# Performance work log

Hardware: AMD Instinct MI355X
Metric: run time of the kernel (lower is better)

## Reference

```python
import jax, jax.numpy as jnp
import numpy as np

S = 14
L_COORD = 5.0
L_NOOBJ = 0.5


def setup_inputs() -> dict:
    key = jax.random.key(0)
    k1, k2, k3, k4 = jax.random.split(key, 4)
    N = 4096
    # positive uniforms so sqrt(w), sqrt(h) and IoU areas are well-defined (as in real YOLO outputs)
    pred_tensor = jax.random.uniform(k1, (N, S, S, 30), dtype=jnp.float32, minval=0.01, maxval=1.0)
    target_boxes = jax.random.uniform(k2, (N, S, S, 4), dtype=jnp.float32, minval=0.01, maxval=1.0)
    target_cls = jax.random.uniform(k3, (N, S, S, 20), dtype=jnp.float32)
    has_object_map = jax.random.bernoulli(k4, 0.15, (N, S, S))
    return {"pred_tensor": pred_tensor, "target_boxes": target_boxes,
            "target_cls": target_cls, "has_object_map": has_object_map}


def _xywh2xyxy(b):
    # b: (..., 4) as [cx, cy, w, h]; cx,cy are in grid units -> divide by S
    x, y, w, h = b[..., 0], b[..., 1], b[..., 2], b[..., 3]
    return jnp.stack([x / S - 0.5 * w, y / S - 0.5 * h,
                      x / S + 0.5 * w, y / S + 0.5 * h], axis=-1)


def _iou_pairwise(b1, b2):
    # elementwise IoU between matched boxes (diag of compute_iou), b: (..., 4) xyxy
    lt = jnp.maximum(b1[..., :2], b2[..., :2])
    rb = jnp.minimum(b1[..., 2:], b2[..., 2:])
    wh = jnp.maximum(rb - lt, 0.0)
    inter = wh[..., 0] * wh[..., 1]
    a1 = (b1[..., 2] - b1[..., 0]) * (b1[..., 3] - b1[..., 1])
    a2 = (b2[..., 2] - b2[..., 0]) * (b2[..., 3] - b2[..., 1])
    return inter / (a1 + a2 - inter)


def reference(pred_tensor, target_boxes, target_cls, has_object_map):
    N = pred_tensor.shape[0]
    obj = has_object_map.astype(pred_tensor.dtype)          # (N,S,S)
    noobj = 1.0 - obj

    box1 = pred_tensor[..., 0:5]
    box2 = pred_tensor[..., 5:10]
    pred_cls = pred_tensor[..., 10:]

    # class loss: masked sum-MSE over object cells
    cls_loss = jnp.sum(obj[..., None] * (pred_cls - target_cls) ** 2)

    # no-object loss: confidences of both predictors in non-object cells vs 0
    no_obj_loss = L_NOOBJ * jnp.sum(noobj * (box1[..., 4] ** 2 + box2[..., 4] ** 2))

    # best-of-B selection by IoU against target (elementwise, matched per cell)
    tgt_xyxy = _xywh2xyxy(target_boxes)
    iou1 = _iou_pairwise(_xywh2xyxy(box1[..., :4]), tgt_xyxy)
    iou2 = _iou_pairwise(_xywh2xyxy(box2[..., :4]), tgt_xyxy)
    take1 = iou1 > iou2
    best_iou = jnp.where(take1, iou1, iou2)                  # (N,S,S)
    best_box = jnp.where(take1[..., None], box1, box2)       # (N,S,S,5)

    xy_err = jnp.sum((best_box[..., :2] - target_boxes[..., :2]) ** 2, axis=-1)
    wh_err = jnp.sum((jnp.sqrt(best_box[..., 2:4]) - jnp.sqrt(target_boxes[..., 2:4])) ** 2, axis=-1)
    reg_loss = L_COORD * jnp.sum(obj * (xy_err + wh_err))

    # containing-object confidence loss; target IoU is detached
    contain_loss = jnp.sum(obj * (best_box[..., 4] - jax.lax.stop_gradient(best_iou)) ** 2)

    total = cls_loss + no_obj_loss + contain_loss + reg_loss
    # [total, reg, containing_obj, no_obj, cls], each averaged over batch
    return jnp.stack([total, reg_loss, contain_loss, no_obj_loss, cls_loss]) / N
```

## Files before the change

kernel.cpp:

```cpp
#include <hip/hip_runtime.h>


#define NBATCH   4096
#define SGRID    14
#define CELLS    (NBATCH * SGRID * SGRID)
#define CPB      256
#define NBLK     (CELLS / CPB)
#define L_COORD  5.0f
#define L_NOOBJ  0.5f

__global__ __launch_bounds__(256) void yolo_main(
    const float* __restrict__ pred,
    const float* __restrict__ tbox,
    const float* __restrict__ tcls,
    const int*   __restrict__ objmap,
    float4*      __restrict__ part)
{
    __shared__ float lds_pred[CPB * 30];
    __shared__ float lds_obj[CPB];
    __shared__ float red[4][4];

    const int tid  = threadIdx.x;
    const int blk  = blockIdx.x;
    const int base = blk * CPB;

    {
        const float4* p4  = (const float4*)pred + (size_t)blk * (CPB * 30 / 4);
        float4*       lp4 = (float4*)lds_pred;
        for (int i = tid; i < CPB * 30 / 4; i += 256)
            lp4[i] = p4[i];
    }
    lds_obj[tid] = objmap[base + tid] ? 1.0f : 0.0f;
    __syncthreads();

    float acc_reg = 0.f, acc_cont = 0.f, acc_noobj = 0.f, acc_cls = 0.f;

    {
        const float4* c4 = (const float4*)tcls + (size_t)blk * (CPB * 20 / 4);
        for (int i = tid; i < CPB * 20 / 4; i += 256) {
            float4 t  = c4[i];
            int cell  = i / 5;
            int ch0   = (i - cell * 5) * 4;
            float o   = lds_obj[cell];
            const float* pc = &lds_pred[cell * 30 + 10 + ch0];
            float d0 = pc[0] - t.x, d1 = pc[1] - t.y;
            float d2 = pc[2] - t.z, d3 = pc[3] - t.w;
            acc_cls += o * (d0*d0 + d1*d1 + d2*d2 + d3*d3);
        }
    }

    {
        const float* pp = &lds_pred[tid * 30];
        float x1 = pp[0], y1 = pp[1], w1 = pp[2], h1 = pp[3], c1 = pp[4];
        float x2 = pp[5], y2 = pp[6], w2 = pp[7], h2 = pp[8], c2 = pp[9];
        float o  = lds_obj[tid];
        float no = 1.0f - o;
        acc_noobj = no * (c1*c1 + c2*c2);

        float4 tb = ((const float4*)tbox)[base + tid];
        const float invS = 1.0f / 14.0f;

        float txc = tb.x * invS, tyc = tb.y * invS;
        float tx1 = txc - 0.5f * tb.z, ty1 = tyc - 0.5f * tb.w;
        float tx2 = txc + 0.5f * tb.z, ty2 = tyc + 0.5f * tb.w;
        float ta  = (tx2 - tx1) * (ty2 - ty1);

        float ax1 = x1 * invS - 0.5f * w1, ay1 = y1 * invS - 0.5f * h1;
        float ax2 = x1 * invS + 0.5f * w1, ay2 = y1 * invS + 0.5f * h1;
        float a1  = (ax2 - ax1) * (ay2 - ay1);
        float iw  = fmaxf(fminf(ax2, tx2) - fmaxf(ax1, tx1), 0.f);
        float ih  = fmaxf(fminf(ay2, ty2) - fmaxf(ay1, ty1), 0.f);
        float inter1 = iw * ih;
        float iou1   = inter1 / (a1 + ta - inter1);

        float bx1 = x2 * invS - 0.5f * w2, by1 = y2 * invS - 0.5f * h2;
        float bx2 = x2 * invS + 0.5f * w2, by2 = y2 * invS + 0.5f * h2;
        float a2  = (bx2 - bx1) * (by2 - by1);
        float jw  = fmaxf(fminf(bx2, tx2) - fmaxf(bx1, tx1), 0.f);
        float jh  = fmaxf(fminf(by2, ty2) - fmaxf(by1, ty1), 0.f);
        float inter2 = jw * jh;
        float iou2   = inter2 / (a2 + ta - inter2);

        bool  t1   = iou1 > iou2;
        float bx   = t1 ? x1 : x2,  by = t1 ? y1 : y2;
        float bw   = t1 ? w1 : w2,  bh = t1 ? h1 : h2;
        float bc   = t1 ? c1 : c2;
        float biou = t1 ? iou1 : iou2;

        float dx = bx - tb.x, dy = by - tb.y;
        float dw = sqrtf(bw) - sqrtf(tb.z);
        float dh = sqrtf(bh) - sqrtf(tb.w);
        acc_reg  = o * (dx*dx + dy*dy + dw*dw + dh*dh);
        float dc = bc - biou;
        acc_cont = o * dc * dc;
    }

    #pragma unroll
    for (int off = 32; off > 0; off >>= 1) {
        acc_reg   += __shfl_down(acc_reg,   off);
        acc_cont  += __shfl_down(acc_cont,  off);
        acc_noobj += __shfl_down(acc_noobj, off);
        acc_cls   += __shfl_down(acc_cls,   off);
    }
    const int wave = tid >> 6, lane = tid & 63;
    if (lane == 0) {
        red[wave][0] = acc_reg;
        red[wave][1] = acc_cont;
        red[wave][2] = acc_noobj;
        red[wave][3] = acc_cls;
    }
    __syncthreads();
    if (tid == 0) {
        float4 p;
        p.x = red[0][0] + red[1][0] + red[2][0] + red[3][0];
        p.y = red[0][1] + red[1][1] + red[2][1] + red[3][1];
        p.z = red[0][2] + red[1][2] + red[2][2] + red[3][2];
        p.w = red[0][3] + red[1][3] + red[2][3] + red[3][3];
        part[blk] = p;
    }
}

__global__ __launch_bounds__(1024) void yolo_reduce(
    const float4* __restrict__ part, float* __restrict__ out)
{
    __shared__ float red[16][4];
    float r = 0.f, c = 0.f, n = 0.f, cl = 0.f;
    for (int i = threadIdx.x; i < NBLK; i += 1024) {
        float4 p = part[i];
        r += p.x; c += p.y; n += p.z; cl += p.w;
    }
    #pragma unroll
    for (int off = 32; off > 0; off >>= 1) {
        r  += __shfl_down(r,  off);
        c  += __shfl_down(c,  off);
        n  += __shfl_down(n,  off);
        cl += __shfl_down(cl, off);
    }
    const int wave = threadIdx.x >> 6, lane = threadIdx.x & 63;
    if (lane == 0) {
        red[wave][0] = r; red[wave][1] = c; red[wave][2] = n; red[wave][3] = cl;
    }
    __syncthreads();
    if (threadIdx.x == 0) {
        float R = 0.f, C = 0.f, Nn = 0.f, Cl = 0.f;
        #pragma unroll
        for (int w = 0; w < 16; ++w) {
            R += red[w][0]; C += red[w][1]; Nn += red[w][2]; Cl += red[w][3];
        }
        const float invN = 1.0f / (float)NBATCH;
        float reg   = L_COORD * R  * invN;
        float cont  =           C  * invN;
        float noobj = L_NOOBJ * Nn * invN;
        float cls   =           Cl * invN;
        out[0] = reg + cont + noobj + cls;
        out[1] = reg;
        out[2] = cont;
        out[3] = noobj;
        out[4] = cls;
    }
}

extern "C" void kernel_launch(void* const* d_in, const int* in_sizes, int n_in,
                              void* d_out, int out_size, void* d_ws, size_t ws_size,
                              hipStream_t stream) {
    const float* pred   = (const float*)d_in[0];
    const float* tbox   = (const float*)d_in[1];
    const float* tcls   = (const float*)d_in[2];
    const int*   objmap = (const int*)  d_in[3];
    float4* part = (float4*)d_ws;
    float*  out  = (float*)d_out;

    yolo_main<<<NBLK, 256, 0, stream>>>(pred, tbox, tcls, objmap, part);
    yolo_reduce<<<1, 1024, 0, stream>>>(part, out);
}
```

Baseline: 209.0 us.

## Drop LDS staging, read cells directly with 4 cells per thread

Each thread now loads its cell's 30 prediction floats directly from global memory as float2 values instead of staging the block's predictions in LDS, and computes class loss per cell instead of per float4 of class targets. The grid shrinks to 784 blocks with each thread handling 4 cells strided across the grid, and the reduce kernel reads one partial per thread. This removes the LDS copy, the barrier and the divide-by-5 indexing, but per-thread loads with a 120-byte stride are less coalesced than the previous contiguous block copy.

```diff
diff --git a/kernel.cpp b/kernel.cpp
--- a/kernel.cpp
+++ b/kernel.cpp
@@ -2,63 +2,55 @@
 
 
 #define NBATCH   4096
-#define SGRID    14
-#define CELLS    (NBATCH * SGRID * SGRID)
-#define CPB      256
-#define NBLK     (CELLS / CPB)
+#define CELLS    (NBATCH * 14 * 14)
+#define THREADS  256
+#define NBLK     784
+#define CPT      4
+#define TSTRIDE  (NBLK * THREADS)
 #define L_COORD  5.0f
 #define L_NOOBJ  0.5f
 
-__global__ __launch_bounds__(256) void yolo_main(
+__global__ __launch_bounds__(THREADS, 8) void yolo_main(
     const float* __restrict__ pred,
     const float* __restrict__ tbox,
     const float* __restrict__ tcls,
     const int*   __restrict__ objmap,
     float4*      __restrict__ part)
 {
-    __shared__ float lds_pred[CPB * 30];
-    __shared__ float lds_obj[CPB];
-    __shared__ float red[4][4];
-
-    const int tid  = threadIdx.x;
-    const int blk  = blockIdx.x;
-    const int base = blk * CPB;
-
-    {
-        const float4* p4  = (const float4*)pred + (size_t)blk * (CPB * 30 / 4);
-        float4*       lp4 = (float4*)lds_pred;
-        for (int i = tid; i < CPB * 30 / 4; i += 256)
-            lp4[i] = p4[i];
-    }
-    lds_obj[tid] = objmap[base + tid] ? 1.0f : 0.0f;
-    __syncthreads();
+    const int tid = threadIdx.x;
+    const int g0  = blockIdx.x * THREADS + tid;
 
     float acc_reg = 0.f, acc_cont = 0.f, acc_noobj = 0.f, acc_cls = 0.f;
+    const float invS = 1.0f / 14.0f;
 
-    {
-        const float4* c4 = (const float4*)tcls + (size_t)blk * (CPB * 20 / 4);
-        for (int i = tid; i < CPB * 20 / 4; i += 256) {
-            float4 t  = c4[i];
-            int cell  = i / 5;
-            int ch0   = (i - cell * 5) * 4;
-            float o   = lds_obj[cell];
-            const float* pc = &lds_pred[cell * 30 + 10 + ch0];
-            float d0 = pc[0] - t.x, d1 = pc[1] - t.y;
-            float d2 = pc[2] - t.z, d3 = pc[3] - t.w;
-            acc_cls += o * (d0*d0 + d1*d1 + d2*d2 + d3*d3);
+    #pragma unroll
+    for (int it = 0; it < CPT; ++it) {
+        const int c = g0 + it * TSTRIDE;
+
+        const float2* p2 = (const float2*)pred + (size_t)c * 15;
+        float2 f0 = p2[0], f1 = p2[1], f2 = p2[2], f3 = p2[3], f4 = p2[4];
+        float4 tb = ((const float4*)tbox)[c];
+        float  o  = objmap[c] ? 1.0f : 0.0f;
+
+        {
+            const float4* t4 = (const float4*)tcls + (size_t)c * 5;
+            float cl = 0.f;
+            #pragma unroll
+            for (int j = 0; j < 5; ++j) {
+                float4 t  = t4[j];
+                float2 a  = p2[5 + 2 * j];
+                float2 b  = p2[6 + 2 * j];
+                float d0 = a.x - t.x, d1 = a.y - t.y;
+                float d2 = b.x - t.z, d3 = b.y - t.w;
+                cl += d0 * d0 + d1 * d1 + d2 * d2 + d3 * d3;
+            }
+            acc_cls += o * cl;
         }
-    }
 
-    {
-        const float* pp = &lds_pred[tid * 30];
-        float x1 = pp[0], y1 = pp[1], w1 = pp[2], h1 = pp[3], c1 = pp[4];
-        float x2 = pp[5], y2 = pp[6], w2 = pp[7], h2 = pp[8], c2 = pp[9];
-        float o  = lds_obj[tid];
-        float no = 1.0f - o;
-        acc_noobj = no * (c1*c1 + c2*c2);
+        float x1 = f0.x, y1 = f0.y, w1 = f1.x, h1 = f1.y, c1 = f2.x;
+        float x2 = f2.y, y2 = f3.x, w2 = f3.y, h2 = f4.x, c2 = f4.y;
 
-        float4 tb = ((const float4*)tbox)[base + tid];
-        const float invS = 1.0f / 14.0f;
+        acc_noobj += (1.0f - o) * (c1 * c1 + c2 * c2);
 
         float txc = tb.x * invS, tyc = tb.y * invS;
         float tx1 = txc - 0.5f * tb.z, ty1 = tyc - 0.5f * tb.w;
@@ -90,11 +82,12 @@
         float dx = bx - tb.x, dy = by - tb.y;
         float dw = sqrtf(bw) - sqrtf(tb.z);
         float dh = sqrtf(bh) - sqrtf(tb.w);
-        acc_reg  = o * (dx*dx + dy*dy + dw*dw + dh*dh);
-        float dc = bc - biou;
-        acc_cont = o * dc * dc;
+        acc_reg  += o * (dx * dx + dy * dy + dw * dw + dh * dh);
+        float dc  = bc - biou;
+        acc_cont += o * dc * dc;
     }
 
+    __shared__ float red[4][4];
     #pragma unroll
     for (int off = 32; off > 0; off >>= 1) {
         acc_reg   += __shfl_down(acc_reg,   off);
@@ -116,7 +109,7 @@
         p.y = red[0][1] + red[1][1] + red[2][1] + red[3][1];
         p.z = red[0][2] + red[1][2] + red[2][2] + red[3][2];
         p.w = red[0][3] + red[1][3] + red[2][3] + red[3][3];
-        part[blk] = p;
+        part[blockIdx.x] = p;
     }
 }
 
@@ -125,9 +118,9 @@
 {
     __shared__ float red[16][4];
     float r = 0.f, c = 0.f, n = 0.f, cl = 0.f;
-    for (int i = threadIdx.x; i < NBLK; i += 1024) {
-        float4 p = part[i];
-        r += p.x; c += p.y; n += p.z; cl += p.w;
+    if (threadIdx.x < NBLK) {
+        float4 p = part[threadIdx.x];
+        r = p.x; c = p.y; n = p.z; cl = p.w;
     }
     #pragma unroll
     for (int off = 32; off > 0; off >>= 1) {
@@ -170,6 +163,6 @@
     float4* part = (float4*)d_ws;
     float*  out  = (float*)d_out;
 
-    yolo_main<<<NBLK, 256, 0, stream>>>(pred, tbox, tcls, objmap, part);
+    yolo_main<<<NBLK, THREADS, 0, stream>>>(pred, tbox, tcls, objmap, part);
     yolo_reduce<<<1, 1024, 0, stream>>>(part, out);
 }
```

Measured after the change: 222.2 us. +6.3%, slower.

## Assign one thread per predictor box and halve cells per block

Applied to the files above, without the earlier changes.

Each block now handles 128 cells with 256 threads. Each thread computes the IoU for one of the two predictor boxes, and the pair exchanges IoUs via a shuffle to pick the winner. LDS per block shrinks and the grid doubles, which is meant to raise occupancy and memory-level parallelism on this bandwidth-bound loss. The cost is duplicated target-box loads, a branch on the winning lane, and twice as many partials for the final reduction.

```diff
diff --git a/kernel.cpp b/kernel.cpp
--- a/kernel.cpp
+++ b/kernel.cpp
@@ -2,14 +2,14 @@
 
 
 #define NBATCH   4096
-#define SGRID    14
-#define CELLS    (NBATCH * SGRID * SGRID)
-#define CPB      256
+#define CELLS    (NBATCH * 14 * 14)
+#define THREADS  256
+#define CPB      128
 #define NBLK     (CELLS / CPB)
 #define L_COORD  5.0f
 #define L_NOOBJ  0.5f
 
-__global__ __launch_bounds__(256) void yolo_main(
+__global__ __launch_bounds__(THREADS, 8) void yolo_main(
     const float* __restrict__ pred,
     const float* __restrict__ tbox,
     const float* __restrict__ tcls,
@@ -27,17 +27,19 @@
     {
         const float4* p4  = (const float4*)pred + (size_t)blk * (CPB * 30 / 4);
         float4*       lp4 = (float4*)lds_pred;
-        for (int i = tid; i < CPB * 30 / 4; i += 256)
+        #pragma unroll
+        for (int i = tid; i < CPB * 30 / 4; i += THREADS)
             lp4[i] = p4[i];
     }
-    lds_obj[tid] = objmap[base + tid] ? 1.0f : 0.0f;
+    if (tid < CPB) lds_obj[tid] = objmap[base + tid] ? 1.0f : 0.0f;
     __syncthreads();
 
     float acc_reg = 0.f, acc_cont = 0.f, acc_noobj = 0.f, acc_cls = 0.f;
 
     {
         const float4* c4 = (const float4*)tcls + (size_t)blk * (CPB * 20 / 4);
-        for (int i = tid; i < CPB * 20 / 4; i += 256) {
+        #pragma unroll
+        for (int i = tid; i < CPB * 20 / 4; i += THREADS) {
             float4 t  = c4[i];
             int cell  = i / 5;
             int ch0   = (i - cell * 5) * 4;
@@ -50,14 +52,15 @@
     }
 
     {
-        const float* pp = &lds_pred[tid * 30];
-        float x1 = pp[0], y1 = pp[1], w1 = pp[2], h1 = pp[3], c1 = pp[4];
-        float x2 = pp[5], y2 = pp[6], w2 = pp[7], h2 = pp[8], c2 = pp[9];
-        float o  = lds_obj[tid];
-        float no = 1.0f - o;
-        acc_noobj = no * (c1*c1 + c2*c2);
+        const int cell = tid >> 1;
+        const int box  = tid & 1;
+        const float* pp = &lds_pred[cell * 30 + box * 5];
+        float x = pp[0], y = pp[1], w = pp[2], h = pp[3], conf = pp[4];
+        float o  = lds_obj[cell];
 
-        float4 tb = ((const float4*)tbox)[base + tid];
+        acc_noobj = (1.0f - o) * conf * conf;
+
+        float4 tb = ((const float4*)tbox)[base + cell];
         const float invS = 1.0f / 14.0f;
 
         float txc = tb.x * invS, tyc = tb.y * invS;
@@ -65,34 +68,25 @@
         float tx2 = txc + 0.5f * tb.z, ty2 = tyc + 0.5f * tb.w;
         float ta  = (tx2 - tx1) * (ty2 - ty1);
 
-        float ax1 = x1 * invS - 0.5f * w1, ay1 = y1 * invS - 0.5f * h1;
-        float ax2 = x1 * invS + 0.5f * w1, ay2 = y1 * invS + 0.5f * h1;
+        float ax1 = x * invS - 0.5f * w, ay1 = y * invS - 0.5f * h;
+        float ax2 = x * invS + 0.5f * w, ay2 = y * invS + 0.5f * h;
         float a1  = (ax2 - ax1) * (ay2 - ay1);
         float iw  = fmaxf(fminf(ax2, tx2) - fmaxf(ax1, tx1), 0.f);
         float ih  = fmaxf(fminf(ay2, ty2) - fmaxf(ay1, ty1), 0.f);
-        float inter1 = iw * ih;
-        float iou1   = inter1 / (a1 + ta - inter1);
+        float inter = iw * ih;
+        float iou   = inter / (a1 + ta - inter);
 
-        float bx1 = x2 * invS - 0.5f * w2, by1 = y2 * invS - 0.5f * h2;
-        float bx2 = x2 * invS + 0.5f * w2, by2 = y2 * invS + 0.5f * h2;
-        float a2  = (bx2 - bx1) * (by2 - by1);
-        float jw  = fmaxf(fminf(bx2, tx2) - fmaxf(bx1, tx1), 0.f);
-        float jh  = fmaxf(fminf(by2, ty2) - fmaxf(by1, ty1), 0.f);
-        float inter2 = jw * jh;
-        float iou2   = inter2 / (a2 + ta - inter2);
+        float iou_other = __shfl_xor(iou, 1);
+        bool win = (box == 0) ? (iou > iou_other) : !(iou_other > iou);
 
-        bool  t1   = iou1 > iou2;
-        float bx   = t1 ? x1 : x2,  by = t1 ? y1 : y2;
-        float bw   = t1 ? w1 : w2,  bh = t1 ? h1 : h2;
-        float bc   = t1 ? c1 : c2;
-        float biou = t1 ? iou1 : iou2;
-
-        float dx = bx - tb.x, dy = by - tb.y;
-        float dw = sqrtf(bw) - sqrtf(tb.z);
-        float dh = sqrtf(bh) - sqrtf(tb.w);
-        acc_reg  = o * (dx*dx + dy*dy + dw*dw + dh*dh);
-        float dc = bc - biou;
-        acc_cont = o * dc * dc;
+        if (win) {
+            float dx = x - tb.x, dy = y - tb.y;
+            float dw = sqrtf(w) - sqrtf(tb.z);
+            float dh = sqrtf(h) - sqrtf(tb.w);
+            acc_reg  = o * (dx*dx + dy*dy + dw*dw + dh*dh);
+            float dc = conf - iou;
+            acc_cont = o * dc * dc;
+        }
     }
 
     #pragma unroll
@@ -170,6 +164,6 @@
     float4* part = (float4*)d_ws;
     float*  out  = (float*)d_out;
 
-    yolo_main<<<NBLK, 256, 0, stream>>>(pred, tbox, tcls, objmap, part);
+    yolo_main<<<NBLK, THREADS, 0, stream>>>(pred, tbox, tcls, objmap, part);
     yolo_reduce<<<1, 1024, 0, stream>>>(part, out);
 }
```

Result: no change. 207.7 us (-0.6%).
